# Optimization experiments

Measured on AMD Instinct MI355X. Metric: run time of the kernel, lower is better.

## Reference

```python
import jax, jax.numpy as jnp
import numpy as np

# Grid config derived from module constants:
# point_cloud_range=[0,-25.6,-2,51.2,25.6,4.4], occ_size=[256,256,32], lss_downsample=[2,2,2]
DX = jnp.array([0.4, 0.4, 0.4], dtype=jnp.float32)
BX = jnp.array([0.2, -25.4, -1.8], dtype=jnp.float32)
NX = (128, 128, 16)  # (x, y, z) voxel counts


def setup_inputs() -> dict:
    key = jax.random.key(0)
    k1, k2, k3 = jax.random.split(key, 3)
    B, N, D, H, W, C = 2, 1, 40, 64, 128, 64  # fH=grd_h//4, fW=grd_w//4, D=40 depth bins
    img_feats = jax.random.normal(k1, (B * N, C, H, W), dtype=jnp.float32)
    depth_logits = jax.random.normal(k2, (B * N, D, H, W), dtype=jnp.float32)
    lo = jnp.array([0.0, -25.6, -2.0], dtype=jnp.float32)
    hi = jnp.array([51.2, 25.6, 4.4], dtype=jnp.float32)
    u = jax.random.uniform(k3, (B, N, D, H, W, 3), dtype=jnp.float32)
    geom = lo + u * (hi - lo)  # ego-frame 3D points of each frustum cell
    return {"img_feats": img_feats, "depth_logits": depth_logits, "geom": geom}


def reference(img_feats, depth_logits, geom):
    B, N, D, H, W, _ = geom.shape
    C = img_feats.shape[1]
    nx_x, nx_y, nx_z = NX

    # ---- LSS lift: depth-distribution-weighted outer product ----
    depth = jax.nn.softmax(depth_logits, axis=1)               # [BN, D, H, W]
    lifted = depth[:, None] * img_feats[:, :, None]            # [BN, C, D, H, W]
    x = lifted.reshape(B, N, C, D, H, W).transpose(0, 1, 3, 4, 5, 2)  # [B,N,D,H,W,C]

    # ---- voxel pooling (splat): scatter-add into BEV/3D grid ----
    Nprime = B * N * D * H * W
    xf = x.reshape(Nprime, C)
    coords = jnp.floor((geom.reshape(Nprime, 3) - (BX - DX / 2.0)) / DX).astype(jnp.int32)
    batch_ix = jnp.repeat(jnp.arange(B, dtype=jnp.int32), N * D * H * W)

    nx_arr = jnp.array(NX, dtype=jnp.int32)
    kept = jnp.all((coords >= 0) & (coords < nx_arr), axis=1)  # in-grid mask

    # linear index: ((b*Z + z)*X + x)*Y + y  -> grid layout [B, Z, X, Y]
    lin = ((batch_ix * nx_z + coords[:, 2]) * nx_x + coords[:, 0]) * nx_y + coords[:, 1]
    lin = jnp.where(kept, lin, 0)
    xf = jnp.where(kept[:, None], xf, 0.0)

    pooled = jax.ops.segment_sum(xf, lin, num_segments=B * nx_z * nx_x * nx_y)  # [B*Z*X*Y, C]

    # final grid [B, C, Z, X, Y]; cat(unbind(dim=2), 1) -> [B, Z*C, X, Y]
    final = pooled.reshape(B, nx_z, nx_x, nx_y, C).transpose(0, 1, 4, 2, 3)  # [B, Z, C, X, Y]
    out = final.reshape(B, nx_z * C, nx_x, nx_y)
    return out
```

## Files before the change

### kernel.cpp

```cpp
#include <hip/hip_runtime.h>
#include <cstddef>

#define BB 2
#define NN 1
#define DD 40
#define HH 64
#define WW 128
#define CC 64
#define GX 128
#define GY 128
#define GZ 16
#define XY (GX * GY)
#define VOX (BB * GZ * GX * GY)
#define KSLOT 16

__global__ __launch_bounds__(256) void lss_tfeat(
    const float* __restrict__ img, float* __restrict__ featT,
    uint4* __restrict__ count4) {
  __shared__ float tile[64][65];
  const int bn = blockIdx.x >> 7;
  const int p0 = (blockIdx.x & 127) << 6;
  const int t = threadIdx.x;

  {
    int base = blockIdx.x * 512 + t;
    count4[base] = make_uint4(0, 0, 0, 0);
    count4[base + 256] = make_uint4(0, 0, 0, 0);
  }

  const float* src = img + (size_t)bn * CC * (HH * WW);
#pragma unroll
  for (int i = 0; i < 4; ++i) {
    int idx = i * 256 + t;
    int r = idx >> 4;
    int c4 = idx & 15;
    float4 v = *(const float4*)(src + (size_t)r * (HH * WW) + p0 + c4 * 4);
    tile[r][c4 * 4 + 0] = v.x;
    tile[r][c4 * 4 + 1] = v.y;
    tile[r][c4 * 4 + 2] = v.z;
    tile[r][c4 * 4 + 3] = v.w;
  }
  __syncthreads();
  float* dst = featT + ((size_t)bn * (HH * WW) + p0) * CC;
#pragma unroll
  for (int i = 0; i < 4; ++i) {
    int idx = i * 256 + t;
    int p = idx >> 4;
    int q = idx & 15;
    float4 v;
    v.x = tile[q * 4 + 0][p];
    v.y = tile[q * 4 + 1][p];
    v.z = tile[q * 4 + 2][p];
    v.w = tile[q * 4 + 3][p];
    *(float4*)(dst + (size_t)p * CC + q * 4) = v;
  }
}

__global__ __launch_bounds__(256) void lss_bin(
    const float* __restrict__ logits, const float* __restrict__ geom,
    unsigned int* __restrict__ count, uint2* __restrict__ rec) {
  const int gtid = blockIdx.x * blockDim.x + threadIdx.x;
  const int pix = gtid >> 6;
  const int lane = threadIdx.x & 63;
  if (pix >= BB * NN * HH * WW) return;
  const int w = pix & (WW - 1);
  const int h = (pix >> 7) & (HH - 1);
  const int bn = pix >> 13;

  float logit = -3.0e38f;
  if (lane < DD) logit = logits[((bn * DD + lane) * HH + h) * WW + w];
  float m = logit;
#pragma unroll
  for (int off = 32; off > 0; off >>= 1) m = fmaxf(m, __shfl_xor(m, off));
  float e = (lane < DD) ? __expf(logit - m) : 0.0f;
  float s = e;
#pragma unroll
  for (int off = 32; off > 0; off >>= 1) s += __shfl_xor(s, off);
  const float dep = e / s;

  if (lane < DD) {
    size_t gb = ((size_t)((bn * DD + lane) * HH + h) * WW + w) * 3;
    float fx = (geom[gb + 0] - 0.0f) / 0.4f;
    float fy = (geom[gb + 1] + 25.6f) / 0.4f;
    float fz = (geom[gb + 2] + 2.0f) / 0.4f;
    int cx = (int)floorf(fx);
    int cy = (int)floorf(fy);
    int cz = (int)floorf(fz);
    if (cx >= 0 && cx < GX && cy >= 0 && cy < GY && cz >= 0 && cz < GZ) {
      int b = bn / NN;
      int v = ((b * GZ + cz) * GX + cx) * GY + cy;
      unsigned int slot = atomicAdd(&count[v], 1u);
      if (slot < KSLOT)
        rec[(size_t)slot * VOX + v] = make_uint2((unsigned)pix, __float_as_uint(dep));
    }
  }
}

__global__ __launch_bounds__(256) void lss_gather(
    const unsigned int* __restrict__ count, const uint2* __restrict__ rec,
    const float* __restrict__ featT, float* __restrict__ out) {
  __shared__ float accs[CC][65];
  __shared__ uint2 recs[KSLOT][64];
  __shared__ unsigned int cnts[64];
  const int t = threadIdx.x;
  const int v0 = blockIdx.x << 6;

  if (t < 64) {
    unsigned int c = count[v0 + t];
    cnts[t] = c > KSLOT ? KSLOT : c;
  }
  __syncthreads();

  {
    const int y = t & 63;
    const int cn = (int)cnts[y];
    for (int s = (t >> 6); s < KSLOT; s += 4)
      if (s < cn) recs[s][y] = rec[(size_t)s * VOX + v0 + y];
  }
  __syncthreads();

  const int lane = t & 63;
  const int wid = t >> 6;
  const int y0 = wid * 16;

  float a[16];
  int cn[16];
#pragma unroll
  for (int i = 0; i < 16; ++i) {
    a[i] = 0.0f;
    cn[i] = (int)cnts[y0 + i];
  }
  int maxcn = 0;
#pragma unroll
  for (int i = 0; i < 16; ++i) maxcn = cn[i] > maxcn ? cn[i] : maxcn;

  for (int s = 0; s < maxcn; ++s) {
    float f[16], w[16];
#pragma unroll
    for (int i = 0; i < 16; ++i) {
      if (s < cn[i]) {
        uint2 r = recs[s][y0 + i];
        w[i] = __uint_as_float(r.y);
        f[i] = featT[(size_t)r.x * CC + lane];
      }
    }
#pragma unroll
    for (int i = 0; i < 16; ++i)
      if (s < cn[i]) a[i] += w[i] * f[i];
  }

#pragma unroll
  for (int i = 0; i < 16; ++i) accs[lane][y0 + i] = a[i];
  __syncthreads();

  const int slab = v0 >> 14;
  const int xy = v0 & (XY - 1);
#pragma unroll
  for (int pass = 0; pass < 4; ++pass) {
    const int c = pass * 16 + (t >> 4);
    const int q = t & 15;
    float4 v;
    v.x = accs[c][q * 4 + 0];
    v.y = accs[c][q * 4 + 1];
    v.z = accs[c][q * 4 + 2];
    v.w = accs[c][q * 4 + 3];
    *(float4*)(out + ((size_t)slab * CC + c) * XY + xy + q * 4) = v;
  }
}

__global__ __launch_bounds__(256) void lss_scatter_direct(
    const float* __restrict__ img, const float* __restrict__ logits,
    const float* __restrict__ geom, float* __restrict__ acc) {
  const int gtid = blockIdx.x * blockDim.x + threadIdx.x;
  const int pix = gtid >> 6;
  const int lane = threadIdx.x & 63;
  if (pix >= BB * NN * HH * WW) return;
  const int w = pix & (WW - 1);
  const int h = (pix >> 7) & (HH - 1);
  const int bn = pix >> 13;

  float logit = -3.0e38f;
  if (lane < DD) logit = logits[((bn * DD + lane) * HH + h) * WW + w];
  float m = logit;
#pragma unroll
  for (int off = 32; off > 0; off >>= 1) m = fmaxf(m, __shfl_xor(m, off));
  float e = (lane < DD) ? __expf(logit - m) : 0.0f;
  float s = e;
#pragma unroll
  for (int off = 32; off > 0; off >>= 1) s += __shfl_xor(s, off);
  const float dep = e / s;

  int base = -1;
  if (lane < DD) {
    size_t gb = ((size_t)((bn * DD + lane) * HH + h) * WW + w) * 3;
    float fx = (geom[gb + 0] - 0.0f) / 0.4f;
    float fy = (geom[gb + 1] + 25.6f) / 0.4f;
    float fz = (geom[gb + 2] + 2.0f) / 0.4f;
    int cx = (int)floorf(fx);
    int cy = (int)floorf(fy);
    int cz = (int)floorf(fz);
    if (cx >= 0 && cx < GX && cy >= 0 && cy < GY && cz >= 0 && cz < GZ) {
      int b = bn / NN;
      base = ((b * GZ + cz) * CC) * XY + cx * GY + cy;
    }
  }
  const float feat = img[((bn * CC + lane) * HH + h) * WW + w];
  for (int d = 0; d < DD; ++d) {
    int bd = __shfl(base, d);
    if (bd >= 0) {
      float wd = __shfl(dep, d);
      atomicAdd(&acc[bd + lane * XY], wd * feat);
    }
  }
}

extern "C" void kernel_launch(void* const* d_in, const int* in_sizes, int n_in,
                              void* d_out, int out_size, void* d_ws, size_t ws_size,
                              hipStream_t stream) {
  const float* img = (const float*)d_in[0];
  const float* logits = (const float*)d_in[1];
  const float* geom = (const float*)d_in[2];
  float* out = (float*)d_out;

  const size_t countBytes = (size_t)VOX * sizeof(unsigned int);
  const size_t recBytes = (size_t)KSLOT * VOX * sizeof(uint2);
  const size_t featTBytes = (size_t)BB * NN * HH * WW * CC * sizeof(float);
  const size_t need = countBytes + recBytes + featTBytes;

  const int pixels = BB * NN * HH * WW;
  const int pixBlocks = (pixels * 64 + 255) / 256;

  if (ws_size >= need) {
    unsigned int* count = (unsigned int*)d_ws;
    uint2* rec = (uint2*)((char*)d_ws + countBytes);
    float* featT = (float*)((char*)d_ws + countBytes + recBytes);

    lss_tfeat<<<BB * NN * (HH * WW / 64), 256, 0, stream>>>(img, featT, (uint4*)count);
    lss_bin<<<pixBlocks, 256, 0, stream>>>(logits, geom, count, rec);
    lss_gather<<<VOX / 64, 256, 0, stream>>>(count, rec, featT, out);
  } else {
    hipMemsetAsync(out, 0, (size_t)BB * GZ * XY * CC * sizeof(float), stream);
    lss_scatter_direct<<<pixBlocks, 256, 0, stream>>>(img, logits, geom, out);
  }
}
```

Baseline: 212.7 us.

## Map one thread per pixel in binning kernel, looping over depth bins

The binning kernel now assigns one thread per pixel instead of one 64-lane wavefront per pixel with 24 idle lanes. Each thread loads all 40 logits into registers, computes the softmax serially without shuffles, and loops over depth bins to bin geometry and append records. Adjacent threads now read adjacent pixels, so logit loads coalesce. The cost is higher register pressure, only 256 single-wave blocks, and strided geom reads per thread.

```diff
diff --git a/kernel.cpp b/kernel.cpp
--- a/kernel.cpp
+++ b/kernel.cpp
@@ -56,42 +56,48 @@
   }
 }
 
-__global__ __launch_bounds__(256) void lss_bin(
+__global__ __launch_bounds__(64) void lss_bin(
     const float* __restrict__ logits, const float* __restrict__ geom,
     unsigned int* __restrict__ count, uint2* __restrict__ rec) {
-  const int gtid = blockIdx.x * blockDim.x + threadIdx.x;
-  const int pix = gtid >> 6;
-  const int lane = threadIdx.x & 63;
-  if (pix >= BB * NN * HH * WW) return;
+  const int t = threadIdx.x;
+  const int pix = blockIdx.x * 64 + t;
   const int w = pix & (WW - 1);
   const int h = (pix >> 7) & (HH - 1);
   const int bn = pix >> 13;
 
-  float logit = -3.0e38f;
-  if (lane < DD) logit = logits[((bn * DD + lane) * HH + h) * WW + w];
-  float m = logit;
-#pragma unroll
-  for (int off = 32; off > 0; off >>= 1) m = fmaxf(m, __shfl_xor(m, off));
-  float e = (lane < DD) ? __expf(logit - m) : 0.0f;
-  float s = e;
-#pragma unroll
-  for (int off = 32; off > 0; off >>= 1) s += __shfl_xor(s, off);
-  const float dep = e / s;
-
-  if (lane < DD) {
-    size_t gb = ((size_t)((bn * DD + lane) * HH + h) * WW + w) * 3;
-    float fx = (geom[gb + 0] - 0.0f) / 0.4f;
-    float fy = (geom[gb + 1] + 25.6f) / 0.4f;
-    float fz = (geom[gb + 2] + 2.0f) / 0.4f;
-    int cx = (int)floorf(fx);
-    int cy = (int)floorf(fy);
-    int cz = (int)floorf(fz);
+  float lg[DD];
+  const float* lp = logits + ((size_t)bn * DD * HH + h) * WW + w;
+#pragma unroll
+  for (int d = 0; d < DD; ++d) lg[d] = lp[(size_t)d * (HH * WW)];
+
+  float m = lg[0];
+#pragma unroll
+  for (int d = 1; d < DD; ++d) m = fmaxf(m, lg[d]);
+  float s = 0.0f;
+#pragma unroll
+  for (int d = 0; d < DD; ++d) {
+    lg[d] = __expf(lg[d] - m);
+    s += lg[d];
+  }
+  const float inv = 1.0f / s;
+
+  const float* gp = geom + ((size_t)(bn * DD * HH + h) * WW + w) * 3;
+#pragma unroll 8
+  for (int d = 0; d < DD; ++d) {
+    const size_t gb = (size_t)d * (HH * WW * 3);
+    float gx = gp[gb + 0];
+    float gy = gp[gb + 1];
+    float gz = gp[gb + 2];
+    int cx = (int)floorf((gx - 0.0f) / 0.4f);
+    int cy = (int)floorf((gy + 25.6f) / 0.4f);
+    int cz = (int)floorf((gz + 2.0f) / 0.4f);
     if (cx >= 0 && cx < GX && cy >= 0 && cy < GY && cz >= 0 && cz < GZ) {
       int b = bn / NN;
       int v = ((b * GZ + cz) * GX + cx) * GY + cy;
       unsigned int slot = atomicAdd(&count[v], 1u);
       if (slot < KSLOT)
-        rec[(size_t)slot * VOX + v] = make_uint2((unsigned)pix, __float_as_uint(dep));
+        rec[(size_t)slot * VOX + v] =
+            make_uint2((unsigned)pix, __float_as_uint(lg[d] * inv));
     }
   }
 }
@@ -228,7 +234,6 @@
   const size_t need = countBytes + recBytes + featTBytes;
 
   const int pixels = BB * NN * HH * WW;
-  const int pixBlocks = (pixels * 64 + 255) / 256;
 
   if (ws_size >= need) {
     unsigned int* count = (unsigned int*)d_ws;
@@ -236,10 +241,10 @@
     float* featT = (float*)((char*)d_ws + countBytes + recBytes);
 
     lss_tfeat<<<BB * NN * (HH * WW / 64), 256, 0, stream>>>(img, featT, (uint4*)count);
-    lss_bin<<<pixBlocks, 256, 0, stream>>>(logits, geom, count, rec);
+    lss_bin<<<pixels / 64, 64, 0, stream>>>(logits, geom, count, rec);
     lss_gather<<<VOX / 64, 256, 0, stream>>>(count, rec, featT, out);
   } else {
     hipMemsetAsync(out, 0, (size_t)BB * GZ * XY * CC * sizeof(float), stream);
-    lss_scatter_direct<<<pixBlocks, 256, 0, stream>>>(img, logits, geom, out);
-  }
-}
+    lss_scatter_direct<<<(pixels * 64 + 255) / 256, 256, 0, stream>>>(img, logits, geom, out);
+  }
+}
```

Result: slower. 247.2 us (+16.2%).
